# Performance work log

Measured on AMD Instinct MI355X. Metric: run time of the kernel, lower is better.

## Reference

```python
import jax, jax.numpy as jnp
import numpy as np
from jax import lax


def _instance_loss(z1, z2, t):
    # z1, z2: [B,T,C]; t: [B,T] timestamps
    B, T, C = z1.shape
    if B == 1:
        return jnp.asarray(0.0, z1.dtype)
    N = B * T
    tf = t.reshape(N)
    diff = jnp.abs(tf[:, None] - tf[None, :])          # [N,N]
    seq = jnp.repeat(jnp.arange(B), T)                 # sequence id per row
    same_seq = seq[:, None] == seq[None, :]
    diff = jnp.where(same_seq, diff + diff.max() + 0.001, diff)
    # k=B smallest diffs per row (cross-sequence temporal neighbors)
    _, idx = lax.top_k(-diff, B)                       # [N,B]
    z1f = z1.reshape(N, C)
    z2f = z2.reshape(N, C)
    pos = jnp.sum(z1f * z2f, axis=-1)[:, None]         # [N,1]
    neg1 = jnp.einsum('nc,nkc->nk', z1f, z1f[idx])     # [N,B]
    neg2 = jnp.einsum('nc,nkc->nk', z1f, z2f[idx])     # [N,B]
    logits = jnp.concatenate([pos, neg1, neg2], axis=1)
    return -jax.nn.log_softmax(logits, axis=1)[:, 0].mean()


def _temporal_loss(z1, z2):
    B, T, C = z1.shape
    if T == 1:
        return jnp.asarray(0.0, z1.dtype)
    z = jnp.concatenate([z1, z2], axis=1)              # [B,2T,C]
    n = 2 * T
    sim = jnp.einsum('bic,bjc->bij', z, z)             # [B,2T,2T]
    # tril(sim,-1)[:,:,:-1] + triu(sim,1)[:,:,1:] == drop-diagonal shift
    i = jnp.arange(n)[:, None]
    j = jnp.arange(n - 1)[None, :]
    logits = jnp.where(j < i, sim[:, :, : n - 1], sim[:, :, 1:])  # [B,2T,2T-1]
    nls = -jax.nn.log_softmax(logits, axis=-1)
    tt = jnp.arange(T)
    return (nls[:, tt, T + tt - 1].mean() + nls[:, T + tt, tt].mean()) / 2


def _max_pool2(z):
    # F.max_pool1d(kernel=2, stride=2) over time axis (floor, drops odd tail)
    B, T, C = z.shape
    T2 = T // 2
    return z[:, : 2 * T2].reshape(B, T2, 2, C).max(axis=2)


def hierarchical_contrastive_loss(z1, z2, t, alpha=0.5, temporal_unit=0):
    B = z1.shape[0]
    loss = jnp.asarray(0.0, z1.dtype)
    d = 0
    while z1.shape[1] > 1:
        if alpha != 0:
            loss = loss + alpha * _instance_loss(z1, z2, t)
        if d >= temporal_unit and (1 - alpha) != 0:
            loss = loss + (1 - alpha) * _temporal_loss(z1, z2)
        d += 1
        z1 = _max_pool2(z1)
        z2 = _max_pool2(z2)
        Tt = t.shape[1]
        if Tt % 2 != 0:
            t = t[:, :-1]
        t = t.reshape(B, -1, 2).mean(axis=2)
    if z1.shape[1] == 1:
        if alpha != 0:
            loss = loss + alpha * _instance_loss(z1, z2, t)
        d += 1
    return loss / d


def setup_inputs() -> dict:
    key = jax.random.key(0)
    k1, k2, k3 = jax.random.split(key, 3)
    B, T, C = 8, 512, 320
    z1 = jax.random.normal(k1, (B, T, C), dtype=jnp.float32)
    z2 = jax.random.normal(k2, (B, T, C), dtype=jnp.float32)
    # irregular, increasing timestamps per sequence
    t = jnp.sort(jax.random.uniform(k3, (B, T), dtype=jnp.float32) * T, axis=1)
    return {"z1": z1, "z2": z2, "t": t}


def reference(z1, z2, t):
    return hierarchical_contrastive_loss(z1, z2, t, alpha=0.5, temporal_unit=0)
```

## Files before the change

### kernel.cpp

```cpp
#include <hip/hip_runtime.h>
#include <math.h>

#define BB 8
#define CC 320
#define ZB 2618880
#define TTOT 4088
#define NROWS 8184
#define NROWS_T 16352
#define NTBLK 440
#define NP1V 81920
#define NP2 5120
#define NMRB 256

#define FT 2618880
#define FPART 2622968
#define FCROSS 2799032
#define FROW 2807208
#define FBLK 2815396
#define FCNT 2815652

constexpr int kT[10]       = {512,256,128,64,32,16,8,4,2,1};
constexpr int kLogT[10]    = {9,8,7,6,5,4,3,2,1,0};
constexpr int kZBoff[10]   = {0,1310720,1966080,2293760,2457600,2539520,2580480,2600960,2611200,2616320};
constexpr int kToff[10]    = {0,0,2048,3072,3584,3840,3968,4032,4064,4080};
constexpr int kRowcum[11]  = {0,4096,6144,7168,7680,7936,8064,8128,8160,8176,8184};
constexpr int kTRowcum[10] = {0,8192,12288,14336,15360,15872,16128,16256,16320,16352};
constexpr int kNt128[9]    = {8,4,2,1,1,1,1,1,1};
constexpr int kLog128[9]   = {3,2,1,0,0,0,0,0,0};
constexpr int kPoff128[9]  = {0,65536,81920,86016,87040,87552,87808,87936,88000};
constexpr int kSblkcum[10] = {0,288,368,392,400,408,416,424,432,440};
constexpr int kXoff[9]     = {0,4096,6144,7168,7680,7936,8064,8128,8160};

typedef short v8s __attribute__((ext_vector_type(8)));
typedef float v16f __attribute__((ext_vector_type(16)));

__device__ __forceinline__ unsigned short f2bf(float x) {
    unsigned int u = __float_as_uint(x);
    u = (u + 0x7FFFu + ((u >> 16) & 1u)) >> 16;
    return (unsigned short)u;
}
__device__ __forceinline__ float bfu(unsigned short u) {
    return __uint_as_float(((unsigned int)u) << 16);
}
__device__ __forceinline__ float4 fmax4(float4 a, float4 b) {
    return make_float4(fmaxf(a.x, b.x), fmaxf(a.y, b.y), fmaxf(a.z, b.z),
                       fmaxf(a.w, b.w));
}
__device__ __forceinline__ ushort4 bf4(float4 v) {
    return make_ushort4(f2bf(v.x), f2bf(v.y), f2bf(v.z), f2bf(v.w));
}

__global__ void pool03_kernel(const float* __restrict__ z1,
                              const float* __restrict__ z2,
                              const float* __restrict__ t,
                              unsigned short* __restrict__ zb,
                              float* __restrict__ tpool,
                              int* __restrict__ counter) {
    int gid = blockIdx.x * 256 + threadIdx.x;
    if (gid == 0) *counter = 0;
    if (gid < NP1V) {
        int c4 = (gid % 80) * 4;
        int rest = gid / 80;
        int ch = rest & 63;
        int b = (rest >> 6) & 7;
        int which = rest >> 9;
        const float* src =
            (which ? z2 : z1) + ((size_t)(b * 512 + ch * 8)) * CC + c4;
        unsigned short* dst = zb + (size_t)which * ZB;
        float4 v[8];
#pragma unroll
        for (int j = 0; j < 8; j++)
            v[j] = *(const float4*)(src + (size_t)j * CC);
#pragma unroll
        for (int j = 0; j < 8; j++)
            *(ushort4*)(dst + (size_t)(b * 512 + ch * 8 + j) * CC + c4) =
                bf4(v[j]);
        float4 m1[4];
#pragma unroll
        for (int j = 0; j < 4; j++) m1[j] = fmax4(v[2 * j], v[2 * j + 1]);
#pragma unroll
        for (int j = 0; j < 4; j++)
            *(ushort4*)(dst + kZBoff[1] +
                        (size_t)(b * 256 + ch * 4 + j) * CC + c4) = bf4(m1[j]);
        float4 m2[2] = {fmax4(m1[0], m1[1]), fmax4(m1[2], m1[3])};
#pragma unroll
        for (int j = 0; j < 2; j++)
            *(ushort4*)(dst + kZBoff[2] +
                        (size_t)(b * 128 + ch * 2 + j) * CC + c4) = bf4(m2[j]);
        *(ushort4*)(dst + kZBoff[3] + (size_t)(b * 64 + ch) * CC + c4) =
            bf4(fmax4(m2[0], m2[1]));
    } else if (gid < NP1V + TTOT) {
        int i = gid - NP1V;
        int l = 1;
#pragma unroll
        for (int q = 2; q <= 9; q++) l = (i >= kToff[q]) ? q : l;
        int rem = i - kToff[l];
        int Tl = kT[l];
        int t2 = rem & (Tl - 1);
        int b = rem >> kLogT[l];
        int win = 512 / Tl;
        const float* p = t + b * 512 + t2 * win;
        float s = 0.f;
        for (int j = 0; j < win; j++) s += p[j];
        tpool[kToff[l] + rem] = s * (1.0f / win);
    }
}

__global__ void pool49_kernel(unsigned short* __restrict__ zb) {
    int gid = blockIdx.x * 256 + threadIdx.x;
    if (gid >= NP2) return;
    int c = gid % CC;
    int r2 = gid / CC;
    int b = r2 & 7;
    int which = r2 >> 3;
    unsigned short* base = zb + (size_t)which * ZB;
    const unsigned short* src = base + kZBoff[3] + (size_t)(b * 64) * CC + c;
    float a[32];
#pragma unroll
    for (int j = 0; j < 32; j++)
        a[j] = fmaxf(bfu(src[(size_t)(2 * j) * CC]),
                     bfu(src[(size_t)(2 * j + 1) * CC]));
#pragma unroll
    for (int j = 0; j < 32; j++)
        base[kZBoff[4] + (size_t)(b * 32 + j) * CC + c] = f2bf(a[j]);
#pragma unroll
    for (int j = 0; j < 16; j++) a[j] = fmaxf(a[2 * j], a[2 * j + 1]);
#pragma unroll
    for (int j = 0; j < 16; j++)
        base[kZBoff[5] + (size_t)(b * 16 + j) * CC + c] = f2bf(a[j]);
#pragma unroll
    for (int j = 0; j < 8; j++) a[j] = fmaxf(a[2 * j], a[2 * j + 1]);
#pragma unroll
    for (int j = 0; j < 8; j++)
        base[kZBoff[6] + (size_t)(b * 8 + j) * CC + c] = f2bf(a[j]);
#pragma unroll
    for (int j = 0; j < 4; j++) a[j] = fmaxf(a[2 * j], a[2 * j + 1]);
#pragma unroll
    for (int j = 0; j < 4; j++)
        base[kZBoff[7] + (size_t)(b * 4 + j) * CC + c] = f2bf(a[j]);
#pragma unroll
    for (int j = 0; j < 2; j++) a[j] = fmaxf(a[2 * j], a[2 * j + 1]);
#pragma unroll
    for (int j = 0; j < 2; j++)
        base[kZBoff[8] + (size_t)(b * 2 + j) * CC + c] = f2bf(a[j]);
    base[kZBoff[9] + (size_t)b * CC + c] = f2bf(fmaxf(a[0], a[1]));
}

__global__ void topk_kernel(const unsigned short* __restrict__ zb,
                            const float* __restrict__ t0,
                            const float* __restrict__ tpool,
                            float* __restrict__ rowloss) {
    int wave = threadIdx.x >> 6, lane = threadIdx.x & 63;
    int row = blockIdx.x * 4 + wave;
    if (row >= NROWS) return;
    int l = 0;
#pragma unroll
    for (int q = 1; q <= 9; q++) l = (row >= kRowcum[q]) ? q : l;
    int n = row - kRowcum[l];
    int T = kT[l];
    const float* tt = l ? tpool + kToff[l] : t0;
    int seq = n >> kLogT[l];
    float tn = tt[n];

    int idx8[8];
    if (lane < 8) {
        const float* ts = tt + lane * T;
        bool own = (lane == seq);
        int lo = 0, hi = T;
        while (lo < hi) {
            int mid = (lo + hi) >> 1;
            if (ts[mid] < tn) lo = mid + 1; else hi = mid;
        }
        int il = lo - 1, ih = lo;
        float dl = (il >= 0) ? (tn - ts[il]) : 3.0e38f;
        float dh = (ih < T) ? (ts[ih] - tn) : 3.0e38f;
#pragma unroll
        for (int r = 0; r < 8; r++) {
            bool pickLo = (dl <= dh);
            float dmin = own ? 1.0e12f : (pickLo ? dl : dh);
            int midx = own ? n : (lane * T + (pickLo ? il : ih));
            unsigned long long key =
                ((unsigned long long)__float_as_uint(dmin) << 32) |
                (unsigned int)midx;
            unsigned long long o;
            o = __shfl_xor(key, 1); key = (key < o) ? key : o;
            o = __shfl_xor(key, 2); key = (key < o) ? key : o;
            o = __shfl_xor(key, 4); key = (key < o) ? key : o;
            int widx = (int)(unsigned int)(key & 0xffffffffull);
            idx8[r] = widx;
            if (!own && widx == midx) {
                if (pickLo) { il--; dl = (il >= 0) ? (tn - ts[il]) : 3.0e38f; }
                else        { ih++; dh = (ih < T)  ? (ts[ih] - tn) : 3.0e38f; }
            }
        }
    }

    const unsigned short* z1 = zb + kZBoff[l];
    const unsigned short* z2 = zb + ZB + kZBoff[l];
    const unsigned short* z1n = z1 + (size_t)n * CC;
    const unsigned short* z2n = z2 + (size_t)n * CC;
    float a[5];
#pragma unroll
    for (int j = 0; j < 5; j++) a[j] = bfu(z1n[lane + 64 * j]);
    float part[17];
    {
        float s = 0.f;
#pragma unroll
        for (int j = 0; j < 5; j++) s += a[j] * bfu(z2n[lane + 64 * j]);
        part[0] = s;
    }
#pragma unroll
    for (int k = 0; k < 8; k++) {
        int p = __shfl(idx8[k], 0);
        const unsigned short* r1 = z1 + (size_t)p * CC;
        const unsigned short* r2 = z2 + (size_t)p * CC;
        float s1 = 0.f, s2 = 0.f;
#pragma unroll
        for (int j = 0; j < 5; j++) {
            float av = a[j];
            s1 += av * bfu(r1[lane + 64 * j]);
            s2 += av * bfu(r2[lane + 64 * j]);
        }
        part[1 + k] = s1;
        part[9 + k] = s2;
    }
#pragma unroll
    for (int q = 0; q < 17; q++) {
        float v = part[q];
        for (int off = 32; off > 0; off >>= 1) v += __shfl_xor(v, off);
        part[q] = v;
    }
    if (lane == 0) {
        float m = part[0];
#pragma unroll
        for (int q = 1; q < 17; q++) m = fmaxf(m, part[q]);
        float s = 0.f;
#pragma unroll
        for (int q = 0; q < 17; q++) s += expf(part[q] - m);
        float w = 0.05f / (float)(BB * T);
        rowloss[row] = w * (m + logf(s) - part[0]);
    }
}

__global__ void __launch_bounds__(256) temporal_kernel(
        const unsigned short* __restrict__ zb, float2* __restrict__ part,
        float* __restrict__ crossbuf) {
    __shared__ __align__(16) char smem[16512];
    int bid = blockIdx.x, tid = threadIdx.x;
    int l = 0;
#pragma unroll
    for (int q = 1; q <= 8; q++) l = (bid >= kSblkcum[q]) ? q : l;
    int rem = bid - kSblkcum[l];
    int b = rem & 7;
    int pr = rem >> 3;
    int Tl = kT[l], n = 2 * Tl, lnt = kLog128[l];
    int rt = 0, width = kNt128[l];
    while (pr >= width) { pr -= width; rt++; width--; }
    int ct = rt + pr;
    bool diag = (rt == ct);
    const unsigned short* zb1 = zb + kZBoff[l] + (size_t)b * Tl * CC;
    const unsigned short* zb2 = zb + ZB + kZBoff[l] + (size_t)b * Tl * CC;
    int row0 = rt * 128, col0 = ct * 128;
    int w = tid >> 6, lane = tid & 63;
    unsigned short* As = (unsigned short*)smem;
    unsigned short* Bs = (unsigned short*)(smem + 8192);
    float2* cred = (float2*)smem;

    v16f acc[4];
#pragma unroll
    for (int cs = 0; cs < 4; cs++)
#pragma unroll
        for (int e = 0; e < 16; e++) acc[cs][e] = 0.f;

    int sofq[2]; const unsigned short* srcA[2]; const unsigned short* srcB[2];
    bool vA[2], vB[2];
#pragma unroll
    for (int q = 0; q < 2; q++) {
        int g = q * 256 + tid;
        int r = g & 127, kbb = g >> 7;
        sofq[q] = (r >> 5) * 1024 + (kbb >> 1) * 512 + (kbb & 1) * 256 +
                  (r & 31) * 8;
        int ka = kbb * 8;
        int gr = row0 + r;
        vA[q] = gr < n;
        srcA[q] = vA[q] ? ((gr < Tl) ? zb1 + (size_t)gr * CC + ka
                                     : zb2 + (size_t)(gr - Tl) * CC + ka)
                        : zb1;
        int gc = col0 + r;
        vB[q] = gc < n;
        srcB[q] = vB[q] ? ((gc < Tl) ? zb1 + (size_t)gc * CC + ka
                                     : zb2 + (size_t)(gc - Tl) * CC + ka)
                        : zb1;
    }

    for (int kc = 0; kc < CC; kc += 32) {
#pragma unroll
        for (int q = 0; q < 2; q++) {
            uint4 av = vA[q] ? *(const uint4*)(srcA[q] + kc)
                             : make_uint4(0, 0, 0, 0);
            *(uint4*)(As + sofq[q]) = av;
            if (!diag) {
                uint4 bv = vB[q] ? *(const uint4*)(srcB[q] + kc)
                                 : make_uint4(0, 0, 0, 0);
                *(uint4*)(Bs + sofq[q]) = bv;
            }
        }
        __syncthreads();
        const unsigned short* Ab = As + w * 1024;
        const unsigned short* Bb = diag ? As : Bs;
#pragma unroll
        for (int cc = 0; cc < 2; cc++) {
            v8s af = *(const v8s*)(Ab + cc * 512 + lane * 8);
#pragma unroll
            for (int cs = 0; cs < 4; cs++) {
                v8s bf = *(const v8s*)(Bb + cs * 1024 + cc * 512 + lane * 8);
                acc[cs] = __builtin_amdgcn_mfma_f32_32x32x16_bf16(
                    af, bf, acc[cs], 0, 0, 0);
            }
        }
        __syncthreads();
    }

    int colin = lane & 31;
    int rowhalf = 4 * (lane >> 5);

#pragma unroll
    for (int r = 0; r < 16; r++) {
        int lrow = (r & 3) + 8 * (r >> 2) + rowhalf;
        int grow = row0 + w * 32 + lrow;
        float vals[4];
        float lm = -3.0e38f;
#pragma unroll
        for (int cs = 0; cs < 4; cs++) {
            int gcol = col0 + cs * 32 + colin;
            float v = acc[cs][r];
            if (gcol >= n || gcol == grow) v = -3.0e38f;
            vals[cs] = v;
            lm = fmaxf(lm, v);
        }
#pragma unroll
        for (int off = 1; off < 32; off <<= 1)
            lm = fmaxf(lm, __shfl_xor(lm, off));
        float ls = 0.f;
#pragma unroll
        for (int cs = 0; cs < 4; cs++)
            ls += (vals[cs] > -1.0e38f) ? expf(vals[cs] - lm) : 0.f;
#pragma unroll
        for (int off = 1; off < 32; off <<= 1) ls += __shfl_xor(ls, off);
        if (colin == 0 && grow < n)
            part[kPoff128[l] + ((b * n + grow) << lnt) + ct] =
                make_float2(lm, ls);
    }

    if (ct - rt == (Tl >> 7)) {
#pragma unroll
        for (int r = 0; r < 16; r++) {
            int lrow = (r & 3) + 8 * (r >> 2) + rowhalf;
            int grow = row0 + w * 32 + lrow;
            if (grow < Tl) {
                int cidx = grow + Tl - col0;
                int cs_p = cidx >> 5, colin_p = cidx & 31;
                float cand = 0.f;
#pragma unroll
                for (int cs = 0; cs < 4; cs++)
                    cand += (cs == cs_p && colin == colin_p) ? acc[cs][r] : 0.f;
#pragma unroll
                for (int off = 1; off < 32; off <<= 1)
                    cand += __shfl_xor(cand, off);
                if (colin == 0)
                    crossbuf[kXoff[l] + b * Tl + grow] = cand;
            }
        }
    }

    if (!diag) {
#pragma unroll
        for (int cs = 0; cs < 4; cs++) {
            float m = acc[cs][0];
#pragma unroll
            for (int r = 1; r < 16; r++) m = fmaxf(m, acc[cs][r]);
            float mo = __shfl_xor(m, 32);
            float mm = fmaxf(m, mo);
            float s = 0.f;
#pragma unroll
            for (int r = 0; r < 16; r++) s += expf(acc[cs][r] - mm);
            s += __shfl_xor(s, 32);
            if (lane < 32) cred[w * 128 + cs * 32 + lane] = make_float2(mm, s);
        }
    }
    __syncthreads();
    if (!diag && tid < 128) {
        float2 a0 = cred[0 * 128 + tid], a1 = cred[1 * 128 + tid];
        float2 a2 = cred[2 * 128 + tid], a3 = cred[3 * 128 + tid];
        float M = fmaxf(fmaxf(a0.x, a1.x), fmaxf(a2.x, a3.x));
        float S = a0.y * expf(a0.x - M) + a1.y * expf(a1.x - M) +
                  a2.y * expf(a2.x - M) + a3.y * expf(a3.x - M);
        int gcol = col0 + tid;
        part[kPoff128[l] + ((b * n + gcol) << lnt) + rt] = make_float2(M, S);
    }
}

__device__ __forceinline__ void d_merge_row(
        int row, const float2* __restrict__ part,
        const float* __restrict__ crossbuf, float* local) {
    int l = 0;
#pragma unroll
    for (int q = 1; q <= 8; q++) l = (row >= kTRowcum[q]) ? q : l;
    int r = row - kTRowcum[l];
    int Tl = kT[l], n = 2 * Tl, nt = kNt128[l], lnt = kLog128[l];
    int b = r >> (kLogT[l] + 1);
    int rr = r & (n - 1);
    const float2* p = part + kPoff128[l] + ((size_t)(b * n + rr) << lnt);
    float M = -3.0e38f, S = 0.f;
    for (int k = 0; k < nt; k++) {
        float2 q2 = p[k];
        float nM = fmaxf(M, q2.x);
        S = S * expf(M - nM) + q2.y * expf(q2.x - nM);
        M = nM;
    }
    float cross = crossbuf[kXoff[l] + b * Tl + (rr < Tl ? rr : rr - Tl)];
    float w = 0.025f / (float)(BB * Tl);
    *local += w * (M + logf(S) - cross);
}

__global__ void merge_reduce_kernel(const float2* __restrict__ part,
                                    const float* __restrict__ crossbuf,
                                    const float* __restrict__ rowloss,
                                    float* __restrict__ blockpart,
                                    int* __restrict__ counter,
                                    float* __restrict__ out) {
    __shared__ float redsm[4];
    __shared__ int flag;
    int bid = blockIdx.x, tid = threadIdx.x;
    int wave = tid >> 6, lane = tid & 63;
    float local = 0.f;
    int row = tid * NMRB + bid;
    if (row < NROWS_T) d_merge_row(row, part, crossbuf, &local);
    if (row < NROWS) local += rowloss[row];
#pragma unroll
    for (int off = 32; off > 0; off >>= 1) local += __shfl_xor(local, off);
    if (lane == 0) redsm[wave] = local;
    __syncthreads();
    if (tid == 0) {
        float bs = redsm[0] + redsm[1] + redsm[2] + redsm[3];
        atomicExch(blockpart + bid, bs);
        __threadfence();
        int old = atomicAdd(counter, 1);
        flag = (old == NMRB - 1) ? 1 : 0;
    }
    __syncthreads();
    if (flag) {
        float v = atomicAdd(blockpart + tid, 0.0f);
#pragma unroll
        for (int off = 32; off > 0; off >>= 1) v += __shfl_xor(v, off);
        if (lane == 0) redsm[wave] = v;
        __syncthreads();
        if (tid == 0) out[0] = redsm[0] + redsm[1] + redsm[2] + redsm[3];
    }
}

extern "C" void kernel_launch(void* const* d_in, const int* in_sizes, int n_in,
                              void* d_out, int out_size, void* d_ws,
                              size_t ws_size, hipStream_t stream) {
    const float* z1 = (const float*)d_in[0];
    const float* z2 = (const float*)d_in[1];
    const float* t  = (const float*)d_in[2];
    float* ws = (float*)d_ws;
    unsigned short* zb = (unsigned short*)ws;
    float* tpool = ws + FT;
    float2* part = (float2*)(ws + FPART);
    float* crossbuf = ws + FCROSS;
    float* rowloss = ws + FROW;
    float* blockpart = ws + FBLK;
    int* counter = (int*)(ws + FCNT);
    float* out = (float*)d_out;

    pool03_kernel<<<(NP1V + TTOT + 255) / 256, 256, 0, stream>>>(
        z1, z2, t, zb, tpool, counter);
    pool49_kernel<<<(NP2 + 255) / 256, 256, 0, stream>>>(zb);
    topk_kernel<<<NROWS / 4, 256, 0, stream>>>(zb, t, tpool, rowloss);
    temporal_kernel<<<NTBLK, 256, 0, stream>>>(zb, part, crossbuf);
    merge_reduce_kernel<<<NMRB, 256, 0, stream>>>(part, crossbuf, rowloss,
                                                  blockpart, counter, out);
}
```

Baseline: 110.4 us.

## Fuse topk and temporal kernels into one launch; shrink merge grid

The separate top-k instance-loss kernel and temporal tile kernel are merged into one work kernel that dispatches by block index: the first 440 blocks do temporal tiles and the rest do top-k rows. This removes one launch and lets the two independent workloads run on the GPU at the same time. The merge-reduce kernel now uses 64 blocks with contiguous row indexing instead of 256 strided blocks, which simplifies the final single-wave reduction. The trade-off is that the top-k blocks now carry the temporal kernel's shared memory allocation and launch bounds, which may lower their occupancy.

```diff
diff --git a/kernel.cpp b/kernel.cpp
--- a/kernel.cpp
+++ b/kernel.cpp
@@ -10,14 +10,14 @@
 #define NTBLK 440
 #define NP1V 81920
 #define NP2 5120
-#define NMRB 256
+#define NMRB 64
 
 #define FT 2618880
 #define FPART 2622968
 #define FCROSS 2799032
 #define FROW 2807208
 #define FBLK 2815396
-#define FCNT 2815652
+#define FCNT 2815460
 
 constexpr int kT[10]       = {512,256,128,64,32,16,8,4,2,1};
 constexpr int kLogT[10]    = {9,8,7,6,5,4,3,2,1,0};
@@ -146,13 +146,10 @@
     base[kZBoff[9] + (size_t)b * CC + c] = f2bf(fmaxf(a[0], a[1]));
 }
 
-__global__ void topk_kernel(const unsigned short* __restrict__ zb,
-                            const float* __restrict__ t0,
-                            const float* __restrict__ tpool,
-                            float* __restrict__ rowloss) {
-    int wave = threadIdx.x >> 6, lane = threadIdx.x & 63;
-    int row = blockIdx.x * 4 + wave;
-    if (row >= NROWS) return;
+__device__ __forceinline__ void d_topk_row(
+        int row, const unsigned short* __restrict__ zb,
+        const float* __restrict__ t0, const float* __restrict__ tpool,
+        int lane, float* __restrict__ rowloss) {
     int l = 0;
 #pragma unroll
     for (int q = 1; q <= 9; q++) l = (row >= kRowcum[q]) ? q : l;
@@ -242,11 +239,10 @@
     }
 }
 
-__global__ void __launch_bounds__(256) temporal_kernel(
-        const unsigned short* __restrict__ zb, float2* __restrict__ part,
-        float* __restrict__ crossbuf) {
-    __shared__ __align__(16) char smem[16512];
-    int bid = blockIdx.x, tid = threadIdx.x;
+__device__ __forceinline__ void d_temporal_tile(
+        int bid, const unsigned short* __restrict__ zb,
+        float2* __restrict__ part, float* __restrict__ crossbuf,
+        char* smem, int tid) {
     int l = 0;
 #pragma unroll
     for (int q = 1; q <= 8; q++) l = (bid >= kSblkcum[q]) ? q : l;
@@ -400,6 +396,21 @@
     }
 }
 
+__global__ void __launch_bounds__(256) work_kernel(
+        const unsigned short* __restrict__ zb, const float* __restrict__ t0,
+        const float* __restrict__ tpool, float2* __restrict__ part,
+        float* __restrict__ crossbuf, float* __restrict__ rowloss) {
+    __shared__ __align__(16) char smem[16512];
+    int bid = blockIdx.x, tid = threadIdx.x;
+    if (bid < NTBLK) {
+        d_temporal_tile(bid, zb, part, crossbuf, smem, tid);
+    } else {
+        int wave = tid >> 6, lane = tid & 63;
+        int row = (bid - NTBLK) * 4 + wave;
+        if (row < NROWS) d_topk_row(row, zb, t0, tpool, lane, rowloss);
+    }
+}
+
 __device__ __forceinline__ void d_merge_row(
         int row, const float2* __restrict__ part,
         const float* __restrict__ crossbuf, float* local) {
@@ -432,11 +443,11 @@
     __shared__ float redsm[4];
     __shared__ int flag;
     int bid = blockIdx.x, tid = threadIdx.x;
+    int gid = bid * 256 + tid;
     int wave = tid >> 6, lane = tid & 63;
     float local = 0.f;
-    int row = tid * NMRB + bid;
-    if (row < NROWS_T) d_merge_row(row, part, crossbuf, &local);
-    if (row < NROWS) local += rowloss[row];
+    if (gid < NROWS_T) d_merge_row(gid, part, crossbuf, &local);
+    if (gid < NROWS) local += rowloss[gid];
 #pragma unroll
     for (int off = 32; off > 0; off >>= 1) local += __shfl_xor(local, off);
     if (lane == 0) redsm[wave] = local;
@@ -449,13 +460,11 @@
         flag = (old == NMRB - 1) ? 1 : 0;
     }
     __syncthreads();
-    if (flag) {
+    if (flag && tid < 64) {
         float v = atomicAdd(blockpart + tid, 0.0f);
 #pragma unroll
         for (int off = 32; off > 0; off >>= 1) v += __shfl_xor(v, off);
-        if (lane == 0) redsm[wave] = v;
-        __syncthreads();
-        if (tid == 0) out[0] = redsm[0] + redsm[1] + redsm[2] + redsm[3];
+        if (tid == 0) out[0] = v;
     }
 }
 
@@ -478,8 +487,8 @@
     pool03_kernel<<<(NP1V + TTOT + 255) / 256, 256, 0, stream>>>(
         z1, z2, t, zb, tpool, counter);
     pool49_kernel<<<(NP2 + 255) / 256, 256, 0, stream>>>(zb);
-    topk_kernel<<<NROWS / 4, 256, 0, stream>>>(zb, t, tpool, rowloss);
-    temporal_kernel<<<NTBLK, 256, 0, stream>>>(zb, part, crossbuf);
+    work_kernel<<<NTBLK + NROWS / 4, 256, 0, stream>>>(zb, t, tpool, part,
+                                                       crossbuf, rowloss);
     merge_reduce_kernel<<<NMRB, 256, 0, stream>>>(part, crossbuf, rowloss,
                                                   blockpart, counter, out);
 }
```

Result: no change. 109.1 us (-1.2%).
